# Optimization experiments

Hardware: AMD Instinct MI355X
Metric: run time of the kernel (lower is better)

## Reference

```python
import jax, jax.numpy as jnp
import numpy as np

NUM_EMBEDDING = 1024
EMBEDDING_DIM = 64


def setup_inputs() -> dict:
    key = jax.random.key(0)
    k1, k2 = jax.random.split(key)
    z_e = jax.random.normal(k1, (64, EMBEDDING_DIM, 32, 32), dtype=jnp.float32)
    # nn.Embedding init: uniform(-1/K, 1/K)
    bound = 1.0 / NUM_EMBEDDING
    weight = jax.random.uniform(k2, (NUM_EMBEDDING, EMBEDDING_DIM),
                                dtype=jnp.float32, minval=-bound, maxval=bound)
    return {"z_e": z_e, "weight": weight}


def reference(z_e, weight):
    B, C, H, W = z_e.shape  # C == embedding_dim
    # NCHW -> NHWC -> [N, D]
    z_flat = jnp.transpose(z_e, (0, 2, 3, 1)).reshape(-1, C)
    d = (jnp.sum(z_flat * z_flat, axis=1, keepdims=True)
         - 2.0 * z_flat @ weight.T
         + jnp.sum(weight * weight, axis=1)[None, :])
    indices = jnp.argmin(d, axis=1)          # [N]
    z_q_flat = weight[indices]               # [N, D] gather
    z_q = z_q_flat.reshape(B, H, W, C).transpose(0, 3, 1, 2)
    return z_q
```

## Files before the change

### kernel.cpp

```cpp
#include <hip/hip_runtime.h>
#include <math.h>
#include <limits.h>

#define NUM_CODES 1024
#define DIM 64
#define HW 1024
#define NPTS 65536
#define PTS 32
#define CAP 16
#define W_WINDOW 6.0e-4f

using short8 = __attribute__((ext_vector_type(8))) short;
using f32x4  = __attribute__((ext_vector_type(4))) float;

__device__ __forceinline__ float pairwise_sumsq64(const float* v) {
    float r[8];
#pragma unroll
    for (int j = 0; j < 8; ++j) r[j] = __fmul_rn(v[j], v[j]);
#pragma unroll
    for (int i = 8; i < 64; i += 8) {
#pragma unroll
        for (int j = 0; j < 8; ++j)
            r[j] = __fadd_rn(r[j], __fmul_rn(v[i + j], v[i + j]));
    }
    return __fadd_rn(
        __fadd_rn(__fadd_rn(r[0], r[1]), __fadd_rn(r[2], r[3])),
        __fadd_rn(__fadd_rn(r[4], r[5]), __fadd_rn(r[6], r[7])));
}

__device__ __forceinline__ float replica_d(const float* x, const float* wr,
                                           float t1, float t3k) {
    float acc = 0.0f;
#pragma unroll
    for (int j = 0; j < 64; ++j) acc = __fmaf_rn(x[j], wr[j], acc);
    return __fadd_rn(__fsub_rn(t1, __fmul_rn(2.0f, acc)), t3k);
}

__device__ __forceinline__ unsigned short bf16_rne(float v) {
    unsigned int u = __float_as_uint(v);
    return (unsigned short)((u + 0x7fffu + ((u >> 16) & 1u)) >> 16);
}

__global__ void vq_prep_kernel(const float* __restrict__ w,
                               unsigned short* __restrict__ wneg2hi,
                               float* __restrict__ t3) {
    int k = blockIdx.x * blockDim.x + threadIdx.x;
    if (k >= NUM_CODES) return;
    float row[64];
#pragma unroll
    for (int j = 0; j < 64; ++j) row[j] = w[k * DIM + j];
    t3[k] = pairwise_sumsq64(row);
#pragma unroll
    for (int j = 0; j < 64; ++j) wneg2hi[k * DIM + j] = bf16_rne(-2.0f * row[j]);
}

__global__ __launch_bounds__(256, 2) void vq_main_kernel(
        const float* __restrict__ z,
        const float* __restrict__ w,
        const unsigned short* __restrict__ wneg2hi,
        const float* __restrict__ t3,
        float* __restrict__ out) {
    __shared__ __align__(16) unsigned short s_xhi[PTS * 72];
    __shared__ float s_pmin[4][PTS];
    __shared__ float s_thr[PTS];
    __shared__ int s_list[PTS * CAP];
    __shared__ int s_cnt[PTS];
    __shared__ int s_ovf[PTS];
    __shared__ int s_best[PTS];
    __shared__ float s_wrow[PTS * 65];

    const int tid = threadIdx.x;
    const int lane = tid & 63;
    const int wv = tid >> 6;
    const int n0 = blockIdx.x * PTS;
    const int b = n0 >> 10;
    const int hw0 = n0 & (HW - 1);

    if (tid < PTS) { s_cnt[tid] = 0; s_ovf[tid] = 0; }

    {
        int hw_off = tid & 31;
        int dbase = tid >> 5;
#pragma unroll
        for (int i = 0; i < 8; ++i) {
            int d = dbase + i * 8;
            float v = z[((size_t)(b * 64 + d)) * HW + hw0 + hw_off];
            s_xhi[hw_off * 72 + d] = bf16_rne(v);
        }
    }
    __syncthreads();

    const int col = lane & 15;
    const int q = lane >> 4;

    short8 ah0[2], ah1[2];
#pragma unroll
    for (int at = 0; at < 2; ++at) {
        int arow = at * 16 + col;
        ah0[at] = *(const short8*)&s_xhi[arow * 72 + q * 8];
        ah1[at] = *(const short8*)&s_xhi[arow * 72 + 32 + q * 8];
    }

    const int T0 = wv * 16;

    float m1[2][4], m2[2][4], m3[2][4];
    int i1[2][4], i2[2][4];
#pragma unroll
    for (int at = 0; at < 2; ++at)
#pragma unroll
        for (int r = 0; r < 4; ++r) {
            m1[at][r] = INFINITY; m2[at][r] = INFINITY; m3[at][r] = INFINITY;
            i1[at][r] = 0; i2[at][r] = 0;
        }

#pragma unroll 4
    for (int t = 0; t < 16; ++t) {
        int code = (T0 + t) * 16 + col;
        short8 b0 = *(const short8*)(wneg2hi + code * 64 + q * 8);
        short8 b1 = *(const short8*)(wneg2hi + code * 64 + 32 + q * 8);
        float t3v = t3[code];
        f32x4 cinit = {t3v, t3v, t3v, t3v};
#pragma unroll
        for (int at = 0; at < 2; ++at) {
            f32x4 c = cinit;
            c = __builtin_amdgcn_mfma_f32_16x16x32_bf16(ah0[at], b0, c, 0, 0, 0);
            c = __builtin_amdgcn_mfma_f32_16x16x32_bf16(ah1[at], b1, c, 0, 0, 0);
#pragma unroll
            for (int r = 0; r < 4; ++r) {
                float s = c[r];
                bool lt1 = s < m1[at][r];
                bool lt2 = s < m2[at][r];
                bool lt3 = s < m3[at][r];
                m3[at][r] = lt2 ? m2[at][r] : (lt3 ? s : m3[at][r]);
                m2[at][r] = lt1 ? m1[at][r] : (lt2 ? s : m2[at][r]);
                i2[at][r] = lt1 ? i1[at][r] : (lt2 ? code : i2[at][r]);
                m1[at][r] = lt1 ? s : m1[at][r];
                i1[at][r] = lt1 ? code : i1[at][r];
            }
        }
    }

    {
        float red[2][4];
#pragma unroll
        for (int at = 0; at < 2; ++at)
#pragma unroll
            for (int r = 0; r < 4; ++r) red[at][r] = m1[at][r];
#pragma unroll
        for (int mask = 1; mask <= 8; mask <<= 1)
#pragma unroll
            for (int at = 0; at < 2; ++at)
#pragma unroll
                for (int r = 0; r < 4; ++r)
                    red[at][r] = fminf(red[at][r], __shfl_xor(red[at][r], mask, 64));
        if (col == 0) {
#pragma unroll
            for (int at = 0; at < 2; ++at)
#pragma unroll
                for (int r = 0; r < 4; ++r)
                    s_pmin[wv][at * 16 + q * 4 + r] = red[at][r];
        }
    }
    __syncthreads();

    if (tid < PTS) {
        float m = fminf(fminf(s_pmin[0][tid], s_pmin[1][tid]),
                        fminf(s_pmin[2][tid], s_pmin[3][tid]));
        s_thr[tid] = m + W_WINDOW;
    }
    __syncthreads();

#pragma unroll
    for (int at = 0; at < 2; ++at)
#pragma unroll
        for (int r = 0; r < 4; ++r) {
            int pt = at * 16 + q * 4 + r;
            float thrW = s_thr[pt];
            if (m1[at][r] <= thrW) {
                int idx = atomicAdd(&s_cnt[pt], 1);
                if (idx < CAP) s_list[pt * CAP + idx] = i1[at][r];
            }
            if (m2[at][r] <= thrW) {
                int idx = atomicAdd(&s_cnt[pt], 1);
                if (idx < CAP) s_list[pt * CAP + idx] = i2[at][r];
            }
            if (m3[at][r] <= thrW) s_ovf[pt] = 1;
        }
    __syncthreads();

    {
        int pt = tid >> 3;
        int sl = tid & 7;
        int cnt = s_cnt[pt];
        int ovf = s_ovf[pt] || (cnt > CAP);
        int best;
        if (cnt <= 1 && !ovf) {
            best = s_list[pt * CAP];
        } else {
            float x[64];
#pragma unroll
            for (int j = 0; j < 64; ++j)
                x[j] = z[((size_t)(b * 64 + j)) * HW + hw0 + pt];
            float t1 = pairwise_sumsq64(x);
            float dbest = INFINITY;
            int kbest = INT_MAX;
            if (!ovf) {
                for (int i = sl; i < cnt; i += 8) {
                    int k = s_list[pt * CAP + i];
                    float d = replica_d(x, w + (size_t)k * DIM, t1, t3[k]);
                    if (d < dbest || (d == dbest && k < kbest)) { dbest = d; kbest = k; }
                }
            } else {
                for (int k = sl; k < NUM_CODES; k += 8) {
                    float d = replica_d(x, w + (size_t)k * DIM, t1, t3[k]);
                    if (d < dbest || (d == dbest && k < kbest)) { dbest = d; kbest = k; }
                }
            }
#pragma unroll
            for (int mask = 1; mask <= 4; mask <<= 1) {
                float od = __shfl_xor(dbest, mask, 64);
                int ok = __shfl_xor(kbest, mask, 64);
                if (od < dbest || (od == dbest && ok < kbest)) { dbest = od; kbest = ok; }
            }
            best = kbest;
        }
        if (sl == 0) s_best[pt] = best;
    }
    __syncthreads();

    {
        int pt = tid >> 3;
        int sl = tid & 7;
        int bk = s_best[pt];
        const float4* wr4 = (const float4*)(w + (size_t)bk * DIM);
#pragma unroll
        for (int i = 0; i < 2; ++i) {
            float4 v = wr4[i * 8 + sl];
            int cb = (i * 8 + sl) * 4;
            s_wrow[pt * 65 + cb + 0] = v.x;
            s_wrow[pt * 65 + cb + 1] = v.y;
            s_wrow[pt * 65 + cb + 2] = v.z;
            s_wrow[pt * 65 + cb + 3] = v.w;
        }
    }
    __syncthreads();

    {
        int pt = tid & 31;
        int cb = tid >> 5;
#pragma unroll
        for (int i = 0; i < 8; ++i) {
            int c = cb + i * 8;
            out[((size_t)(b * 64 + c)) * HW + hw0 + pt] = s_wrow[pt * 65 + c];
        }
    }
}

extern "C" void kernel_launch(void* const* d_in, const int* in_sizes, int n_in,
                              void* d_out, int out_size, void* d_ws, size_t ws_size,
                              hipStream_t stream) {
    const float* z = (const float*)d_in[0];
    const float* w = (const float*)d_in[1];
    float* out = (float*)d_out;

    unsigned short* wneg2hi = (unsigned short*)d_ws;
    float* t3 = (float*)((char*)d_ws + 131072);

    vq_prep_kernel<<<NUM_CODES / 256, 256, 0, stream>>>(w, wneg2hi, t3);
    vq_main_kernel<<<NPTS / PTS, 256, 0, stream>>>(z, w, wneg2hi, t3, out);
}
```

Baseline: 61.28 us.

## Replace top-3 tracking with per-lane rescan queue for ambiguous candidates

The MFMA scan now tracks only the best and second-best distance per lane instead of the top three with two indices, which cuts per-element select work in the hot loop. When a lane's second-best falls inside the threshold window, the lane is pushed to a shared queue. The 16 codes it covered are then recomputed from the bf16 data and added to the candidate list if they fall within threshold plus a small epsilon. This avoids the full 1024-code fallback that the old third-min overflow triggered. It adds an extra sync and a scalar recheck phase, and the epsilon could miss candidates near the threshold if bf16 rounding differs from the MFMA path.

```diff
diff --git a/kernel.cpp b/kernel.cpp
--- a/kernel.cpp
+++ b/kernel.cpp
@@ -9,6 +9,8 @@
 #define PTS 32
 #define CAP 16
 #define W_WINDOW 6.0e-4f
+#define RESQ_EPS 2.0e-5f
+#define RESQ_MAX 64
 
 using short8 = __attribute__((ext_vector_type(8))) short;
 using f32x4  = __attribute__((ext_vector_type(4))) float;
@@ -39,6 +41,10 @@
 __device__ __forceinline__ unsigned short bf16_rne(float v) {
     unsigned int u = __float_as_uint(v);
     return (unsigned short)((u + 0x7fffu + ((u >> 16) & 1u)) >> 16);
+}
+
+__device__ __forceinline__ float bf16_to_f32(unsigned short h) {
+    return __uint_as_float(((unsigned int)h) << 16);
 }
 
 __global__ void vq_prep_kernel(const float* __restrict__ w,
@@ -65,9 +71,10 @@
     __shared__ float s_thr[PTS];
     __shared__ int s_list[PTS * CAP];
     __shared__ int s_cnt[PTS];
-    __shared__ int s_ovf[PTS];
     __shared__ int s_best[PTS];
     __shared__ float s_wrow[PTS * 65];
+    __shared__ int s_resq[RESQ_MAX];
+    __shared__ int s_rescnt;
 
     const int tid = threadIdx.x;
     const int lane = tid & 63;
@@ -76,7 +83,8 @@
     const int b = n0 >> 10;
     const int hw0 = n0 & (HW - 1);
 
-    if (tid < PTS) { s_cnt[tid] = 0; s_ovf[tid] = 0; }
+    if (tid < PTS) s_cnt[tid] = 0;
+    if (tid == 0) s_rescnt = 0;
 
     {
         int hw_off = tid & 31;
@@ -103,14 +111,13 @@
 
     const int T0 = wv * 16;
 
-    float m1[2][4], m2[2][4], m3[2][4];
-    int i1[2][4], i2[2][4];
+    float m1[2][4], m2[2][4];
+    int i1[2][4];
 #pragma unroll
     for (int at = 0; at < 2; ++at)
 #pragma unroll
         for (int r = 0; r < 4; ++r) {
-            m1[at][r] = INFINITY; m2[at][r] = INFINITY; m3[at][r] = INFINITY;
-            i1[at][r] = 0; i2[at][r] = 0;
+            m1[at][r] = INFINITY; m2[at][r] = INFINITY; i1[at][r] = 0;
         }
 
 #pragma unroll 4
@@ -130,10 +137,7 @@
                 float s = c[r];
                 bool lt1 = s < m1[at][r];
                 bool lt2 = s < m2[at][r];
-                bool lt3 = s < m3[at][r];
-                m3[at][r] = lt2 ? m2[at][r] : (lt3 ? s : m3[at][r]);
                 m2[at][r] = lt1 ? m1[at][r] : (lt2 ? s : m2[at][r]);
-                i2[at][r] = lt1 ? i1[at][r] : (lt2 ? code : i2[at][r]);
                 m1[at][r] = lt1 ? s : m1[at][r];
                 i1[at][r] = lt1 ? code : i1[at][r];
             }
@@ -181,18 +185,41 @@
                 if (idx < CAP) s_list[pt * CAP + idx] = i1[at][r];
             }
             if (m2[at][r] <= thrW) {
+                int e = atomicAdd(&s_rescnt, 1);
+                if (e < RESQ_MAX) s_resq[e] = pt | (wv << 5) | (col << 7);
+            }
+        }
+    __syncthreads();
+
+    {
+        int rc = s_rescnt;
+        int rcl = rc < RESQ_MAX ? rc : RESQ_MAX;
+        for (int e = tid >> 4; e < rcl; e += 16) {
+            int ent = s_resq[e];
+            int pt = ent & 31;
+            int wvv = (ent >> 5) & 3;
+            int cc = (ent >> 7) & 15;
+            int t = tid & 15;
+            int code = wvv * 256 + t * 16 + cc;
+            const unsigned short* xr = &s_xhi[pt * 72];
+            const unsigned short* wr = wneg2hi + code * 64;
+            float acc = t3[code];
+#pragma unroll
+            for (int j = 0; j < 64; ++j)
+                acc = __fmaf_rn(bf16_to_f32(xr[j]), bf16_to_f32(wr[j]), acc);
+            if (acc <= s_thr[pt] + RESQ_EPS) {
                 int idx = atomicAdd(&s_cnt[pt], 1);
-                if (idx < CAP) s_list[pt * CAP + idx] = i2[at][r];
-            }
-            if (m3[at][r] <= thrW) s_ovf[pt] = 1;
-        }
+                if (idx < CAP) s_list[pt * CAP + idx] = code;
+            }
+        }
+    }
     __syncthreads();
 
     {
         int pt = tid >> 3;
         int sl = tid & 7;
         int cnt = s_cnt[pt];
-        int ovf = s_ovf[pt] || (cnt > CAP);
+        int ovf = (cnt > CAP) || (s_rescnt > RESQ_MAX);
         int best;
         if (cnt <= 1 && !ovf) {
             best = s_list[pt * CAP];
```

After: 55.28 us. -9.8%, faster.
